# Kernel tuning notes

Measured on AMD Instinct MI355X. Metric: run time of the kernel, lower is better.

Reference implementation:

```python
import jax, jax.numpy as jnp
import numpy as np

HIDDEN = 1024

def setup_inputs() -> dict:
    key = jax.random.key(0)
    ks = jax.random.split(key, 7)
    B, S, H = 4, 4096, HIDDEN
    x = jax.random.normal(ks[0], (B, S, H), dtype=jnp.float32)
    s = 1.0 / np.sqrt(H)
    Wq = jax.random.normal(ks[1], (H, H), dtype=jnp.float32) * s
    bq = jnp.zeros((H,), dtype=jnp.float32)
    Wk = jax.random.normal(ks[2], (H, H), dtype=jnp.float32) * s
    bk = jnp.zeros((H,), dtype=jnp.float32)
    Wv = jax.random.normal(ks[3], (H, H), dtype=jnp.float32) * s
    bv = jnp.zeros((H,), dtype=jnp.float32)
    return {"x": x, "Wq": Wq, "bq": bq, "Wk": Wk, "bk": bk, "Wv": Wv, "bv": bv}

def reference(x, Wq, bq, Wk, bk, Wv, bv):
    # x: [B, S, H]
    scale = jnp.sqrt(jnp.asarray(x.shape[-1], dtype=x.dtype))
    q = jnp.einsum('bsh,hd->bsd', x, Wq) + bq
    k = jnp.einsum('bsh,hd->bsd', x, Wk) + bk
    v = jnp.einsum('bsh,hd->bsd', x, Wv) + bv
    energy = jnp.einsum('bqd,bkd->bqk', q, k) / scale  # [B, S, S]
    attn = jax.nn.softmax(energy, axis=-1)
    return jnp.einsum('bqk,bkd->bqd', attn, v)
```

## Files before the change

### kernel.cpp

```cpp
#include <hip/hip_runtime.h>

typedef unsigned short u16;
typedef __attribute__((ext_vector_type(8))) short short8;
typedef __attribute__((ext_vector_type(4))) short short4v;
typedef __attribute__((ext_vector_type(4))) float floatx4;

#define HD 1024
#define SEQ 4096

__device__ inline u16 f2bf(float f) {
    union { float f; unsigned int i; } c; c.f = f;
    unsigned int r = c.i + 0x7fffu + ((c.i >> 16) & 1u);
    return (u16)(r >> 16);
}

__device__ inline float bf2f(u16 h) {
    union { unsigned int u; float f; } c; c.u = ((unsigned int)h) << 16;
    return c.f;
}

__device__ inline int xcd_chunk(int bid, int nwg) {
    int q = nwg >> 3;
    return (bid & 7) * q + (bid >> 3);
}

__global__ __launch_bounds__(256) void cvt_kernel(const float* __restrict__ in,
                                                  u16* __restrict__ out, int n4) {
    int idx = blockIdx.x * 256 + threadIdx.x;
    int stride = gridDim.x * 256;
    for (int i = idx; i < n4; i += stride) {
        floatx4 v = ((const floatx4*)in)[i];
        short4v o;
        o[0] = (short)f2bf(v[0]); o[1] = (short)f2bf(v[1]);
        o[2] = (short)f2bf(v[2]); o[3] = (short)f2bf(v[3]);
        ((short4v*)out)[i] = o;
    }
}

__global__ __launch_bounds__(256) void wt_kernel(const float* __restrict__ Wq,
                                                 const float* __restrict__ Wk,
                                                 const float* __restrict__ Wv,
                                                 u16* __restrict__ wt) {
    __shared__ u16 tile[64 * 65];
    int z = blockIdx.z;
    const float* W = (z == 0) ? Wq : ((z == 1) ? Wk : Wv);
    u16* out = wt + (size_t)z * HD * HD;
    int k0 = blockIdx.x * 64, n0 = blockIdx.y * 64;
    int t = threadIdx.x;
    int r = t >> 4, c4 = (t & 15) * 4;
    for (int h = 0; h < 4; ++h) {
        int row = r + h * 16;
        floatx4 v = *(const floatx4*)(W + (size_t)(k0 + row) * HD + n0 + c4);
        tile[row * 65 + c4 + 0] = f2bf(v[0]);
        tile[row * 65 + c4 + 1] = f2bf(v[1]);
        tile[row * 65 + c4 + 2] = f2bf(v[2]);
        tile[row * 65 + c4 + 3] = f2bf(v[3]);
    }
    __syncthreads();
    int r2 = t >> 3, c8 = (t & 7) * 8;
    union { short8 v; u16 u[8]; } buf;
    for (int h = 0; h < 2; ++h) {
        int rr = r2 + h * 32;
        #pragma unroll
        for (int i = 0; i < 8; ++i) buf.u[i] = tile[(c8 + i) * 65 + rr];
        *(short8*)(out + (size_t)(n0 + rr) * HD + k0 + c8) = buf.v;
    }
}

__global__ __launch_bounds__(256, 2) void qkv_gemm(const u16* __restrict__ x,
                                                   const u16* __restrict__ wt,
                                                   const float* __restrict__ bq,
                                                   const float* __restrict__ bk,
                                                   const float* __restrict__ bv,
                                                   u16* __restrict__ qb,
                                                   u16* __restrict__ kbuf,
                                                   u16* __restrict__ vtb) {
    __shared__ __align__(16) u16 sA[128 * 32];
    __shared__ __align__(16) u16 sB[128 * 32];
    __shared__ __align__(16) u16 tileC[128 * 132];
    int z = blockIdx.z;
    const u16* Bt = wt + (size_t)z * HD * HD;
    const float* bias = (z == 0) ? bq : ((z == 1) ? bk : bv);
    int m0 = blockIdx.x * 128, n0 = blockIdx.y * 128;
    int t = threadIdx.x, lane = t & 63, w = t >> 6;
    int quad = lane >> 4, l16 = lane & 15;
    int wm = w >> 1, wn = w & 1;
    floatx4 acc[4][4] = {};

    int srow = w * 32 + (lane >> 2);
    int sswz = (lane & 3) ^ ((lane >> 3) & 3);
    const u16* gA = x + (size_t)(m0 + srow) * HD + sswz * 8;
    const u16* gB = Bt + (size_t)(n0 + srow) * HD + sswz * 8;
    u16* lA0 = &sA[(w * 32) * 32];
    u16* lA1 = &sA[(w * 32 + 16) * 32];
    u16* lB0 = &sB[(w * 32) * 32];
    u16* lB1 = &sB[(w * 32 + 16) * 32];

    for (int k0 = 0; k0 < HD; k0 += 32) {
        __builtin_amdgcn_global_load_lds(
            (const __attribute__((address_space(1))) unsigned int*)(const void*)(gA + k0),
            (__attribute__((address_space(3))) unsigned int*)(void*)lA0, 16, 0, 0);
        __builtin_amdgcn_global_load_lds(
            (const __attribute__((address_space(1))) unsigned int*)(const void*)(gA + (size_t)16 * HD + k0),
            (__attribute__((address_space(3))) unsigned int*)(void*)lA1, 16, 0, 0);
        __builtin_amdgcn_global_load_lds(
            (const __attribute__((address_space(1))) unsigned int*)(const void*)(gB + k0),
            (__attribute__((address_space(3))) unsigned int*)(void*)lB0, 16, 0, 0);
        __builtin_amdgcn_global_load_lds(
            (const __attribute__((address_space(1))) unsigned int*)(const void*)(gB + (size_t)16 * HD + k0),
            (__attribute__((address_space(3))) unsigned int*)(void*)lB1, 16, 0, 0);
        __syncthreads();
        short8 af[4], bfr[4];
        #pragma unroll
        for (int i = 0; i < 4; ++i) {
            int ra = wm * 64 + i * 16 + l16;
            af[i] = *(const short8*)&sA[ra * 32 + (quad ^ ((ra >> 1) & 3)) * 8];
        }
        #pragma unroll
        for (int j = 0; j < 4; ++j) {
            int rb = wn * 64 + j * 16 + l16;
            bfr[j] = *(const short8*)&sB[rb * 32 + (quad ^ ((rb >> 1) & 3)) * 8];
        }
        #pragma unroll
        for (int i = 0; i < 4; ++i)
            #pragma unroll
            for (int j = 0; j < 4; ++j)
                acc[i][j] = __builtin_amdgcn_mfma_f32_16x16x32_bf16(af[i], bfr[j], acc[i][j], 0, 0, 0);
        __syncthreads();
    }

    #pragma unroll
    for (int j = 0; j < 4; ++j) {
        int nl = wn * 64 + j * 16 + l16;
        float bb = bias[n0 + nl];
        #pragma unroll
        for (int i = 0; i < 4; ++i) {
            #pragma unroll
            for (int rr = 0; rr < 4; ++rr) {
                int ml = wm * 64 + i * 16 + quad * 4 + rr;
                tileC[ml * 132 + nl] = f2bf(acc[i][j][rr] + bb);
            }
        }
    }
    __syncthreads();
    int r = t >> 1, c0 = (t & 1) * 64;
    if (z != 2) {
        u16* dst = (z == 0) ? qb : kbuf;
        #pragma unroll
        for (int v = 0; v < 8; ++v) {
            short8 vv = *(const short8*)&tileC[r * 132 + c0 + v * 8];
            *(short8*)&dst[(size_t)(m0 + r) * HD + n0 + c0 + v * 8] = vv;
        }
    } else {
        int b_ = m0 >> 12, s0 = m0 & 4095;
        #pragma unroll
        for (int v = 0; v < 8; ++v) {
            union { short8 vv; u16 u[8]; } pk;
            #pragma unroll
            for (int e = 0; e < 8; ++e) pk.u[e] = tileC[(c0 + v * 8 + e) * 132 + r];
            *(short8*)&vtb[((size_t)(b_ * HD + n0 + r)) * SEQ + s0 + c0 + v * 8] = pk.vv;
        }
    }
}

template<int LDA, int LDB, int LDC, int KT, int MT, int NT, bool F32OUT>
__global__ __launch_bounds__(512, 2) void gemm256(const u16* __restrict__ A,
                                                  const u16* __restrict__ B,
                                                  void* __restrict__ C,
                                                  float scale) {
    __shared__ __align__(16) u16 ring[4][2][256 * 32];
    constexpr int NWG = 4 * MT * NT;
    int wg = xcd_chunk(blockIdx.x, NWG);
    int b = wg / (MT * NT);
    int r = wg % (MT * NT);
    int m0 = (r / NT) * 256, n0 = (r % NT) * 256;
    const u16* Ab = A + (size_t)b * MT * 256 * LDA;
    const u16* Bb = B + (size_t)b * NT * 256 * LDB;

    int t = threadIdx.x, lane = t & 63, w = t >> 6;
    int quad = lane >> 4, l16 = lane & 15;
    int wm = w >> 2, wn = w & 3;

    int srow = w * 32 + (lane >> 2);
    int sswz = (lane & 3) ^ ((lane >> 3) & 3);
    const u16* gAs = Ab + (size_t)(m0 + srow) * LDA + sswz * 8;
    const u16* gBs = Bb + (size_t)(n0 + srow) * LDB + sswz * 8;

    auto stage = [&](int kt_) {
        int s_ = kt_ & 3;
        const u16* a0 = gAs + (size_t)kt_ * 32;
        const u16* b0 = gBs + (size_t)kt_ * 32;
        u16* dA = &ring[s_][0][(w * 32) * 32];
        u16* dB = &ring[s_][1][(w * 32) * 32];
        __builtin_amdgcn_global_load_lds(
            (const __attribute__((address_space(1))) unsigned int*)(const void*)a0,
            (__attribute__((address_space(3))) unsigned int*)(void*)dA, 16, 0, 0);
        __builtin_amdgcn_global_load_lds(
            (const __attribute__((address_space(1))) unsigned int*)(const void*)(a0 + (size_t)16 * LDA),
            (__attribute__((address_space(3))) unsigned int*)(void*)(dA + 16 * 32), 16, 0, 0);
        __builtin_amdgcn_global_load_lds(
            (const __attribute__((address_space(1))) unsigned int*)(const void*)b0,
            (__attribute__((address_space(3))) unsigned int*)(void*)dB, 16, 0, 0);
        __builtin_amdgcn_global_load_lds(
            (const __attribute__((address_space(1))) unsigned int*)(const void*)(b0 + (size_t)16 * LDB),
            (__attribute__((address_space(3))) unsigned int*)(void*)(dB + 16 * 32), 16, 0, 0);
    };

    stage(0); stage(1); stage(2);

    floatx4 acc[8][4] = {};

    for (int kt = 0; kt < KT; ++kt) {
        if (kt + 2 < KT)       asm volatile("s_waitcnt vmcnt(8)" ::: "memory");
        else if (kt + 2 == KT) asm volatile("s_waitcnt vmcnt(4)" ::: "memory");
        else                   asm volatile("s_waitcnt vmcnt(0)" ::: "memory");
        __builtin_amdgcn_s_barrier();
        asm volatile("" ::: "memory");
        if (kt + 3 < KT) stage(kt + 3);

        const u16* As = &ring[kt & 3][0][0];
        const u16* Bs = &ring[kt & 3][1][0];
        short8 bf[4], af[8];
        #pragma unroll
        for (int j = 0; j < 4; ++j) {
            int rb = wn * 64 + j * 16 + l16;
            bf[j] = *(const short8*)&Bs[rb * 32 + (quad ^ ((rb >> 1) & 3)) * 8];
        }
        #pragma unroll
        for (int i = 0; i < 8; ++i) {
            int ra = wm * 128 + i * 16 + l16;
            af[i] = *(const short8*)&As[ra * 32 + (quad ^ ((ra >> 1) & 3)) * 8];
        }
        __builtin_amdgcn_s_setprio(1);
        #pragma unroll
        for (int i = 0; i < 8; ++i)
            #pragma unroll
            for (int j = 0; j < 4; ++j)
                acc[i][j] = __builtin_amdgcn_mfma_f32_16x16x32_bf16(af[i], bf[j], acc[i][j], 0, 0, 0);
        __builtin_amdgcn_s_setprio(0);
    }

    if constexpr (F32OUT) {
        float* Cb = (float*)C + (size_t)b * MT * 256 * LDC;
        #pragma unroll
        for (int i = 0; i < 8; ++i)
            #pragma unroll
            for (int rr = 0; rr < 4; ++rr) {
                int m = m0 + wm * 128 + i * 16 + quad * 4 + rr;
                float* row = Cb + (size_t)m * LDC + n0 + wn * 64 + l16;
                #pragma unroll
                for (int j = 0; j < 4; ++j)
                    row[j * 16] = acc[i][j][rr] * scale;
            }
    } else {
        u16* Cb = (u16*)C + (size_t)b * MT * 256 * LDC;
        #pragma unroll
        for (int i = 0; i < 8; ++i)
            #pragma unroll
            for (int rr = 0; rr < 4; ++rr) {
                int m = m0 + wm * 128 + i * 16 + quad * 4 + rr;
                u16* row = Cb + (size_t)m * LDC + n0 + wn * 64 + l16;
                #pragma unroll
                for (int j = 0; j < 4; ++j)
                    row[j * 16] = f2bf(acc[i][j][rr] * scale);
            }
    }
}

__global__ __launch_bounds__(256) void softmax_kernel(u16* __restrict__ S) {
    int w = threadIdx.x >> 6, lane = threadIdx.x & 63;
    size_t row = (size_t)blockIdx.x * 4 + w;
    u16* p = S + row * SEQ;
    float sv[64];
    float mx = -1e30f;
    #pragma unroll
    for (int c = 0; c < 8; ++c) {
        short8 v = *(const short8*)&p[(c * 64 + lane) * 8];
        #pragma unroll
        for (int e = 0; e < 8; ++e) {
            float f = bf2f((u16)v[e]);
            sv[c * 8 + e] = f;
            mx = fmaxf(mx, f);
        }
    }
    mx = fmaxf(mx, __shfl_xor(mx, 1));
    mx = fmaxf(mx, __shfl_xor(mx, 2));
    mx = fmaxf(mx, __shfl_xor(mx, 4));
    mx = fmaxf(mx, __shfl_xor(mx, 8));
    mx = fmaxf(mx, __shfl_xor(mx, 16));
    mx = fmaxf(mx, __shfl_xor(mx, 32));
    float sum = 0.f;
    #pragma unroll
    for (int i = 0; i < 64; ++i) { sv[i] = __expf(sv[i] - mx); sum += sv[i]; }
    sum += __shfl_xor(sum, 1);
    sum += __shfl_xor(sum, 2);
    sum += __shfl_xor(sum, 4);
    sum += __shfl_xor(sum, 8);
    sum += __shfl_xor(sum, 16);
    sum += __shfl_xor(sum, 32);
    float rinv = 1.f / sum;
    #pragma unroll
    for (int c = 0; c < 8; ++c) {
        union { short8 vv; u16 u[8]; } o;
        #pragma unroll
        for (int e = 0; e < 8; ++e) o.u[e] = f2bf(sv[c * 8 + e] * rinv);
        *(short8*)&p[(c * 64 + lane) * 8] = o.vv;
    }
}

__global__ __launch_bounds__(512, 2) void flash_kernel(const u16* __restrict__ q,
                                                       const u16* __restrict__ k,
                                                       const u16* __restrict__ vt,
                                                       float* __restrict__ out) {
    __shared__ __align__(16) u16 q_lds[64 * 1032];
    __shared__ float Sc[64 * 66];
    __shared__ __align__(16) u16 Pb[64 * 72];
    __shared__ float m_st[64], l_st[64], al_st[64];

    int t = threadIdx.x, lane = t & 63, w = t >> 6;
    int quad = lane >> 4, l16 = lane & 15;
    int j = w & 3, hh = w >> 2;
    int bid = blockIdx.x;
    int xcd = bid & 7;
    int b = xcd >> 1;
    int q0 = (((bid >> 3) << 1) + (xcd & 1)) * 64;

    for (int i = t; i < 64 * 128; i += 512) {
        int r = i >> 7, c8 = (i & 127) * 8;
        *(short8*)&q_lds[r * 1032 + c8] =
            *(const short8*)&q[((size_t)(b * SEQ + q0 + r)) * HD + c8];
    }
    if (t < 64) { m_st[t] = -1e30f; l_st[t] = 0.f; }
    floatx4 o_acc[4][8] = {};
    __syncthreads();

    const u16* kwave = k + ((size_t)(b * SEQ + j * 16 + l16)) * HD + hh * 512 + quad * 8;
    const u16* vwave = vt + ((size_t)(b * HD + w * 128 + l16)) * SEQ + quad * 8;
    int r2 = t >> 3;
    int cg = (t & 7) * 8;

    for (int tt = 0; tt < 64; ++tt) {
        int kb = tt * 64;
        floatx4 s_acc[4] = {};
        const u16* kp = kwave + (size_t)kb * HD;
        #pragma unroll 8
        for (int ks = 0; ks < 16; ++ks) {
            short8 kf = *(const short8*)(kp + ks * 32);
            #pragma unroll
            for (int rb = 0; rb < 4; ++rb) {
                short8 qf = *(const short8*)&q_lds[(rb * 16 + l16) * 1032 + hh * 512 + ks * 32 + quad * 8];
                s_acc[rb] = __builtin_amdgcn_mfma_f32_16x16x32_bf16(qf, kf, s_acc[rb], 0, 0, 0);
            }
        }
        if (hh == 0) {
            #pragma unroll
            for (int rb = 0; rb < 4; ++rb)
                #pragma unroll
                for (int rr = 0; rr < 4; ++rr)
                    Sc[(rb * 16 + quad * 4 + rr) * 66 + j * 16 + l16] = s_acc[rb][rr] * 0.03125f;
        }
        __syncthreads();
        if (hh == 1) {
            #pragma unroll
            for (int rb = 0; rb < 4; ++rb)
                #pragma unroll
                for (int rr = 0; rr < 4; ++rr)
                    Sc[(rb * 16 + quad * 4 + rr) * 66 + j * 16 + l16] += s_acc[rb][rr] * 0.03125f;
        }
        __syncthreads();

        float sv[8];
        float mloc = -1e30f;
        #pragma unroll
        for (int i = 0; i < 8; ++i) { sv[i] = Sc[r2 * 66 + cg + i]; mloc = fmaxf(mloc, sv[i]); }
        mloc = fmaxf(mloc, __shfl_xor(mloc, 1));
        mloc = fmaxf(mloc, __shfl_xor(mloc, 2));
        mloc = fmaxf(mloc, __shfl_xor(mloc, 4));
        float m_old = m_st[r2];
        float m_new = fmaxf(m_old, mloc);
        float alpha = __expf(m_old - m_new);
        float sum = 0.f;
        #pragma unroll
        for (int i = 0; i < 8; ++i) {
            float p = __expf(sv[i] - m_new);
            sum += p;
            Pb[r2 * 72 + cg + i] = f2bf(p);
        }
        sum += __shfl_xor(sum, 1);
        sum += __shfl_xor(sum, 2);
        sum += __shfl_xor(sum, 4);
        if ((t & 7) == 0) {
            m_st[r2] = m_new;
            l_st[r2] = l_st[r2] * alpha + sum;
            al_st[r2] = alpha;
        }
        __syncthreads();

        #pragma unroll
        for (int rb = 0; rb < 4; ++rb) {
            float a0 = al_st[rb * 16 + quad * 4 + 0];
            float a1 = al_st[rb * 16 + quad * 4 + 1];
            float a2 = al_st[rb * 16 + quad * 4 + 2];
            float a3 = al_st[rb * 16 + quad * 4 + 3];
            #pragma unroll
            for (int dt = 0; dt < 8; ++dt) {
                o_acc[rb][dt][0] *= a0;
                o_acc[rb][dt][1] *= a1;
                o_acc[rb][dt][2] *= a2;
                o_acc[rb][dt][3] *= a3;
            }
        }
        short8 pf[4][2];
        #pragma unroll
        for (int rb = 0; rb < 4; ++rb)
            #pragma unroll
            for (int ks2 = 0; ks2 < 2; ++ks2)
                pf[rb][ks2] = *(const short8*)&Pb[(rb * 16 + l16) * 72 + ks2 * 32 + quad * 8];
        const u16* vp = vwave + kb;
        #pragma unroll
        for (int dt = 0; dt < 8; ++dt) {
            short8 vf0 = *(const short8*)(vp + (size_t)dt * 16 * SEQ);
            short8 vf1 = *(const short8*)(vp + (size_t)dt * 16 * SEQ + 32);
            #pragma unroll
            for (int rb = 0; rb < 4; ++rb) {
                o_acc[rb][dt] = __builtin_amdgcn_mfma_f32_16x16x32_bf16(pf[rb][0], vf0, o_acc[rb][dt], 0, 0, 0);
                o_acc[rb][dt] = __builtin_amdgcn_mfma_f32_16x16x32_bf16(pf[rb][1], vf1, o_acc[rb][dt], 0, 0, 0);
            }
        }
    }

    #pragma unroll
    for (int rb = 0; rb < 4; ++rb) {
        #pragma unroll
        for (int rr = 0; rr < 4; ++rr) {
            int row = rb * 16 + quad * 4 + rr;
            float linv = 1.f / l_st[row];
            #pragma unroll
            for (int dt = 0; dt < 8; ++dt) {
                out[((size_t)(b * SEQ + q0 + row)) * HD + w * 128 + dt * 16 + l16] =
                    o_acc[rb][dt][rr] * linv;
            }
        }
    }
}

extern "C" void kernel_launch(void* const* d_in, const int* in_sizes, int n_in,
                              void* d_out, int out_size, void* d_ws, size_t ws_size,
                              hipStream_t stream) {
    const float* x  = (const float*)d_in[0];
    const float* Wq = (const float*)d_in[1];
    const float* bq = (const float*)d_in[2];
    const float* Wk = (const float*)d_in[3];
    const float* bk = (const float*)d_in[4];
    const float* Wv = (const float*)d_in[5];
    const float* bv = (const float*)d_in[6];
    float* out = (float*)d_out;
    char* ws = (char*)d_ws;
    const size_t MB = 1024 * 1024;

    if (ws_size >= 224 * MB) {
        u16* vtb = (u16*)ws;
        u16* qb  = (u16*)(ws + 32 * MB);
        u16* kb  = (u16*)(ws + 64 * MB);
        u16* S   = (u16*)(ws + 96 * MB);
        u16* xb  = (u16*)(ws + 96 * MB);
        u16* wt  = (u16*)(ws + 128 * MB);

        cvt_kernel<<<dim3(4096), 256, 0, stream>>>(x, xb, (4 * SEQ * HD) / 4);
        wt_kernel<<<dim3(16, 16, 3), 256, 0, stream>>>(Wq, Wk, Wv, wt);
        qkv_gemm<<<dim3(128, 8, 3), 256, 0, stream>>>(xb, wt, bq, bk, bv, qb, kb, vtb);
        gemm256<HD, HD, SEQ, 32, 16, 16, false><<<dim3(1024), 512, 0, stream>>>(qb, kb, S, 0.03125f);
        softmax_kernel<<<dim3(4096), 256, 0, stream>>>(S);
        gemm256<SEQ, SEQ, HD, 128, 16, 4, true><<<dim3(256), 512, 0, stream>>>(S, vtb, out, 1.0f);
    } else {
        u16* xb  = (u16*)ws;
        u16* wt  = (u16*)(ws + 32 * MB);
        u16* qb  = (u16*)(ws + 38 * MB);
        u16* kb  = (u16*)(ws + 70 * MB);
        u16* vtb = (u16*)(ws + 102 * MB);

        cvt_kernel<<<dim3(4096), 256, 0, stream>>>(x, xb, (4 * SEQ * HD) / 4);
        wt_kernel<<<dim3(16, 16, 3), 256, 0, stream>>>(Wq, Wk, Wv, wt);
        qkv_gemm<<<dim3(128, 8, 3), 256, 0, stream>>>(xb, wt, bq, bk, bv, qb, kb, vtb);
        flash_kernel<<<dim3(256), 512, 0, stream>>>(qb, kb, vtb, out);
    }
}
```

Measured before the change: 568.4 us.

## Split QKV projection into 256x256 pipelined Q/K kernel and separate V kernel

```diff
diff --git a/kernel.cpp b/kernel.cpp
--- a/kernel.cpp
+++ b/kernel.cpp
@@ -64,6 +64,180 @@
         #pragma unroll
         for (int i = 0; i < 8; ++i) buf.u[i] = tile[(c8 + i) * 65 + rr];
         *(short8*)(out + (size_t)(n0 + rr) * HD + k0 + c8) = buf.v;
+    }
+}
+
+__global__ __launch_bounds__(512, 2) void qkv256(const u16* __restrict__ x,
+                                                 const u16* __restrict__ wt,
+                                                 const float* __restrict__ bq,
+                                                 const float* __restrict__ bk,
+                                                 u16* __restrict__ qb,
+                                                 u16* __restrict__ kbuf) {
+    __shared__ __align__(16) u16 ring[4][2][256 * 32];
+    int wg = xcd_chunk(blockIdx.x, 512);
+    int z = wg >> 8;
+    int r = wg & 255;
+    int m0 = (r >> 2) * 256, n0 = (r & 3) * 256;
+    const u16* Bb = wt + (size_t)z * HD * HD;
+    const float* bias = z ? bk : bq;
+    u16* C = z ? kbuf : qb;
+
+    int t = threadIdx.x, lane = t & 63, w = t >> 6;
+    int quad = lane >> 4, l16 = lane & 15;
+    int wm = w >> 2, wn = w & 3;
+
+    int srow = w * 32 + (lane >> 2);
+    int sswz = (lane & 3) ^ ((lane >> 3) & 3);
+    const u16* gAs = x + (size_t)(m0 + srow) * HD + sswz * 8;
+    const u16* gBs = Bb + (size_t)(n0 + srow) * HD + sswz * 8;
+
+    auto stage = [&](int kt_) {
+        int s_ = kt_ & 3;
+        const u16* a0 = gAs + (size_t)kt_ * 32;
+        const u16* b0 = gBs + (size_t)kt_ * 32;
+        u16* dA = &ring[s_][0][(w * 32) * 32];
+        u16* dB = &ring[s_][1][(w * 32) * 32];
+        __builtin_amdgcn_global_load_lds(
+            (const __attribute__((address_space(1))) unsigned int*)(const void*)a0,
+            (__attribute__((address_space(3))) unsigned int*)(void*)dA, 16, 0, 0);
+        __builtin_amdgcn_global_load_lds(
+            (const __attribute__((address_space(1))) unsigned int*)(const void*)(a0 + (size_t)16 * HD),
+            (__attribute__((address_space(3))) unsigned int*)(void*)(dA + 16 * 32), 16, 0, 0);
+        __builtin_amdgcn_global_load_lds(
+            (const __attribute__((address_space(1))) unsigned int*)(const void*)b0,
+            (__attribute__((address_space(3))) unsigned int*)(void*)dB, 16, 0, 0);
+        __builtin_amdgcn_global_load_lds(
+            (const __attribute__((address_space(1))) unsigned int*)(const void*)(b0 + (size_t)16 * HD),
+            (__attribute__((address_space(3))) unsigned int*)(void*)(dB + 16 * 32), 16, 0, 0);
+    };
+
+    stage(0); stage(1); stage(2);
+
+    floatx4 acc[8][4] = {};
+    constexpr int KT = HD / 32;
+
+    for (int kt = 0; kt < KT; ++kt) {
+        if (kt + 2 < KT)       asm volatile("s_waitcnt vmcnt(8)" ::: "memory");
+        else if (kt + 2 == KT) asm volatile("s_waitcnt vmcnt(4)" ::: "memory");
+        else                   asm volatile("s_waitcnt vmcnt(0)" ::: "memory");
+        __builtin_amdgcn_s_barrier();
+        asm volatile("" ::: "memory");
+        if (kt + 3 < KT) stage(kt + 3);
+
+        const u16* As = &ring[kt & 3][0][0];
+        const u16* Bs = &ring[kt & 3][1][0];
+        short8 bf[4], af[8];
+        #pragma unroll
+        for (int j = 0; j < 4; ++j) {
+            int rb = wn * 64 + j * 16 + l16;
+            bf[j] = *(const short8*)&Bs[rb * 32 + (quad ^ ((rb >> 1) & 3)) * 8];
+        }
+        #pragma unroll
+        for (int i = 0; i < 8; ++i) {
+            int ra = wm * 128 + i * 16 + l16;
+            af[i] = *(const short8*)&As[ra * 32 + (quad ^ ((ra >> 1) & 3)) * 8];
+        }
+        __builtin_amdgcn_s_setprio(1);
+        #pragma unroll
+        for (int i = 0; i < 8; ++i)
+            #pragma unroll
+            for (int j = 0; j < 4; ++j)
+                acc[i][j] = __builtin_amdgcn_mfma_f32_16x16x32_bf16(af[i], bf[j], acc[i][j], 0, 0, 0);
+        __builtin_amdgcn_s_setprio(0);
+    }
+
+    float bb[4];
+    #pragma unroll
+    for (int j = 0; j < 4; ++j) bb[j] = bias[n0 + wn * 64 + j * 16 + l16];
+    #pragma unroll
+    for (int i = 0; i < 8; ++i)
+        #pragma unroll
+        for (int rr = 0; rr < 4; ++rr) {
+            int m = m0 + wm * 128 + i * 16 + quad * 4 + rr;
+            u16* row = C + (size_t)m * HD + n0 + wn * 64 + l16;
+            #pragma unroll
+            for (int j = 0; j < 4; ++j)
+                row[j * 16] = f2bf(acc[i][j][rr] + bb[j]);
+        }
+}
+
+__global__ __launch_bounds__(256, 2) void v_gemm(const u16* __restrict__ x,
+                                                 const u16* __restrict__ wtv,
+                                                 const float* __restrict__ bv,
+                                                 u16* __restrict__ vtb) {
+    __shared__ __align__(16) u16 sA[128 * 32];
+    __shared__ __align__(16) u16 sB[128 * 32];
+    __shared__ __align__(16) u16 tileC[128 * 132];
+    int m0 = blockIdx.x * 128, n0 = blockIdx.y * 128;
+    int t = threadIdx.x, lane = t & 63, w = t >> 6;
+    int quad = lane >> 4, l16 = lane & 15;
+    int wm = w >> 1, wn = w & 1;
+    floatx4 acc[4][4] = {};
+
+    int srow = w * 32 + (lane >> 2);
+    int sswz = (lane & 3) ^ ((lane >> 3) & 3);
+    const u16* gA = x + (size_t)(m0 + srow) * HD + sswz * 8;
+    const u16* gB = wtv + (size_t)(n0 + srow) * HD + sswz * 8;
+    u16* lA0 = &sA[(w * 32) * 32];
+    u16* lA1 = &sA[(w * 32 + 16) * 32];
+    u16* lB0 = &sB[(w * 32) * 32];
+    u16* lB1 = &sB[(w * 32 + 16) * 32];
+
+    for (int k0 = 0; k0 < HD; k0 += 32) {
+        __builtin_amdgcn_global_load_lds(
+            (const __attribute__((address_space(1))) unsigned int*)(const void*)(gA + k0),
+            (__attribute__((address_space(3))) unsigned int*)(void*)lA0, 16, 0, 0);
+        __builtin_amdgcn_global_load_lds(
+            (const __attribute__((address_space(1))) unsigned int*)(const void*)(gA + (size_t)16 * HD + k0),
+            (__attribute__((address_space(3))) unsigned int*)(void*)lA1, 16, 0, 0);
+        __builtin_amdgcn_global_load_lds(
+            (const __attribute__((address_space(1))) unsigned int*)(const void*)(gB + k0),
+            (__attribute__((address_space(3))) unsigned int*)(void*)lB0, 16, 0, 0);
+        __builtin_amdgcn_global_load_lds(
+            (const __attribute__((address_space(1))) unsigned int*)(const void*)(gB + (size_t)16 * HD + k0),
+            (__attribute__((address_space(3))) unsigned int*)(void*)lB1, 16, 0, 0);
+        __syncthreads();
+        short8 af[4], bfr[4];
+        #pragma unroll
+        for (int i = 0; i < 4; ++i) {
+            int ra = wm * 64 + i * 16 + l16;
+            af[i] = *(const short8*)&sA[ra * 32 + (quad ^ ((ra >> 1) & 3)) * 8];
+        }
+        #pragma unroll
+        for (int j = 0; j < 4; ++j) {
+            int rb = wn * 64 + j * 16 + l16;
+            bfr[j] = *(const short8*)&sB[rb * 32 + (quad ^ ((rb >> 1) & 3)) * 8];
+        }
+        #pragma unroll
+        for (int i = 0; i < 4; ++i)
+            #pragma unroll
+            for (int j = 0; j < 4; ++j)
+                acc[i][j] = __builtin_amdgcn_mfma_f32_16x16x32_bf16(af[i], bfr[j], acc[i][j], 0, 0, 0);
+        __syncthreads();
+    }
+
+    #pragma unroll
+    for (int j = 0; j < 4; ++j) {
+        int nl = wn * 64 + j * 16 + l16;
+        float bb = bv[n0 + nl];
+        #pragma unroll
+        for (int i = 0; i < 4; ++i) {
+            #pragma unroll
+            for (int rr = 0; rr < 4; ++rr) {
+                int ml = wm * 64 + i * 16 + quad * 4 + rr;
+                tileC[ml * 132 + nl] = f2bf(acc[i][j][rr] + bb);
+            }
+        }
+    }
+    __syncthreads();
+    int r = t >> 1, c0 = (t & 1) * 64;
+    int b_ = m0 >> 12, s0 = m0 & 4095;
+    #pragma unroll
+    for (int v = 0; v < 8; ++v) {
+        union { short8 vv; u16 u[8]; } pk;
+        #pragma unroll
+        for (int e = 0; e < 8; ++e) pk.u[e] = tileC[(c0 + v * 8 + e) * 132 + r];
+        *(short8*)&vtb[((size_t)(b_ * HD + n0 + r)) * SEQ + s0 + c0 + v * 8] = pk.vv;
     }
 }
 
@@ -468,7 +642,8 @@
 
         cvt_kernel<<<dim3(4096), 256, 0, stream>>>(x, xb, (4 * SEQ * HD) / 4);
         wt_kernel<<<dim3(16, 16, 3), 256, 0, stream>>>(Wq, Wk, Wv, wt);
-        qkv_gemm<<<dim3(128, 8, 3), 256, 0, stream>>>(xb, wt, bq, bk, bv, qb, kb, vtb);
+        qkv256<<<dim3(512), 512, 0, stream>>>(xb, wt, bq, bk, qb, kb);
+        v_gemm<<<dim3(128, 8), 256, 0, stream>>>(xb, wt + (size_t)2 * HD * HD, bv, vtb);
         gemm256<HD, HD, SEQ, 32, 16, 16, false><<<dim3(1024), 512, 0, stream>>>(qb, kb, S, 0.03125f);
         softmax_kernel<<<dim3(4096), 256, 0, stream>>>(S);
         gemm256<SEQ, SEQ, HD, 128, 16, 4, true><<<dim3(256), 512, 0, stream>>>(S, vtb, out, 1.0f);
```

Measured after the change: 548.4 us. 1.04x faster.

## Rework gemm256 to BK=64 double-buffer with interleaved fragment loads; split QK projection

Applied to the files above, without the earlier changes.

```diff
diff --git a/kernel.cpp b/kernel.cpp
--- a/kernel.cpp
+++ b/kernel.cpp
@@ -22,6 +22,12 @@
 __device__ inline int xcd_chunk(int bid, int nwg) {
     int q = nwg >> 3;
     return (bid & 7) * q + (bid >> 3);
+}
+
+__device__ inline void glds16(const u16* g, u16* l) {
+    __builtin_amdgcn_global_load_lds(
+        (const __attribute__((address_space(1))) unsigned int*)(const void*)g,
+        (__attribute__((address_space(3))) unsigned int*)(void*)l, 16, 0, 0);
 }
 
 __global__ __launch_bounds__(256) void cvt_kernel(const float* __restrict__ in,
@@ -64,6 +70,214 @@
         #pragma unroll
         for (int i = 0; i < 8; ++i) buf.u[i] = tile[(c8 + i) * 65 + rr];
         *(short8*)(out + (size_t)(n0 + rr) * HD + k0 + c8) = buf.v;
+    }
+}
+
+#define RD_A(i, ks) (*(const short8*)&As[(wm * 128 + (i) * 16 + l16) * 64 + ((((ks) * 4 + quad)) ^ (l16 & 7)) * 8])
+#define RD_B(j, ks) (*(const short8*)&Bs[(wn * 64 + (j) * 16 + l16) * 64 + ((((ks) * 4 + quad)) ^ (l16 & 7)) * 8])
+
+#define GEMM256_CORE(KTN, LDA_, LDB_)                                                   \
+    int t = threadIdx.x, lane = t & 63, w = t >> 6;                                     \
+    int quad = lane >> 4, l16 = lane & 15;                                              \
+    int wm = w >> 2, wn = w & 3;                                                        \
+    int l8r = lane >> 3;                                                                \
+    int sswz = (lane & 7) ^ l8r;                                                        \
+    const u16* gAs = Ab + (size_t)(m0 + w * 32 + l8r) * LDA_ + sswz * 8;                \
+    const u16* gBs = Bb + (size_t)(n0 + w * 32 + l8r) * LDB_ + sswz * 8;                \
+    auto stage = [&](int kt_) {                                                         \
+        int s_ = kt_ & 1;                                                               \
+        const u16* a0 = gAs + (size_t)kt_ * 64;                                         \
+        const u16* b0 = gBs + (size_t)kt_ * 64;                                         \
+        _Pragma("unroll")                                                               \
+        for (int L = 0; L < 4; ++L) {                                                   \
+            glds16(a0 + (size_t)(8 * L) * LDA_, &ring[s_][0][(w * 32 + 8 * L) * 64]);   \
+            glds16(b0 + (size_t)(8 * L) * LDB_, &ring[s_][1][(w * 32 + 8 * L) * 64]);   \
+        }                                                                               \
+    };                                                                                  \
+    floatx4 acc[8][4] = {};                                                             \
+    stage(0);                                                                           \
+    for (int kt = 0; kt < (KTN); ++kt) {                                                \
+        asm volatile("s_waitcnt vmcnt(0)" ::: "memory");        \
+        __builtin_amdgcn_s_barrier();                         \
+        asm volatile("" ::: "memory");                                                  \
+        if (kt + 1 < (KTN)) stage(kt + 1);      \
+        const u16* As = &ring[kt & 1][0][0];                                            \
+        const u16* Bs = &ring[kt & 1][1][0];                                            \
+        short8 bfr[2][4];                                                               \
+        short8 afr[2][2];                                                               \
+        _Pragma("unroll")                                                               \
+        for (int j = 0; j < 4; ++j) bfr[0][j] = RD_B(j, 0);                             \
+        afr[0][0] = RD_A(0, 0);                                                         \
+        afr[0][1] = RD_A(1, 0);                                                         \
+        _Pragma("unroll")                                                               \
+        for (int p = 0; p < 8; ++p) {                                                   \
+            int ks = p >> 2, q = p & 3;                                                 \
+            int cur = p & 1, nxt = cur ^ 1;                                             \
+            if (p < 7) {                                                                \
+                int pn = p + 1;                                                         \
+                int ksn = pn >> 2, qn = pn & 3;                                         \
+                if (qn == 0) {                                                          \
+                    _Pragma("unroll")                                                   \
+                    for (int j = 0; j < 4; ++j) bfr[1][j] = RD_B(j, 1);                 \
+                }                                                                       \
+                afr[nxt][0] = RD_A(2 * qn, ksn);                                        \
+                afr[nxt][1] = RD_A(2 * qn + 1, ksn);                                    \
+            }                                                                           \
+            __builtin_amdgcn_s_setprio(1);                                              \
+            _Pragma("unroll")                                                           \
+            for (int j = 0; j < 4; ++j) {                                               \
+                acc[2 * q][j] = __builtin_amdgcn_mfma_f32_16x16x32_bf16(afr[cur][0], bfr[ks][j], acc[2 * q][j], 0, 0, 0);       \
+                acc[2 * q + 1][j] = __builtin_amdgcn_mfma_f32_16x16x32_bf16(afr[cur][1], bfr[ks][j], acc[2 * q + 1][j], 0, 0, 0); \
+            }                                                                           \
+            __builtin_amdgcn_s_setprio(0);                                              \
+        }                                                                               \
+    }
+
+template<int LDA, int LDB, int LDC, int KT, int MT, int NT, bool F32OUT>
+__global__ __launch_bounds__(512, 2) void gemm256(const u16* __restrict__ A,
+                                                  const u16* __restrict__ B,
+                                                  void* __restrict__ C,
+                                                  float scale) {
+    __shared__ __align__(16) u16 ring[2][2][256 * 64];
+    constexpr int NWG = 4 * MT * NT;
+    int wg = xcd_chunk(blockIdx.x, NWG);
+    int b = wg / (MT * NT);
+    int r = wg % (MT * NT);
+    int m0 = (r / NT) * 256, n0 = (r % NT) * 256;
+    const u16* Ab = A + (size_t)b * MT * 256 * LDA;
+    const u16* Bb = B + (size_t)b * NT * 256 * LDB;
+
+    GEMM256_CORE(KT, LDA, LDB)
+
+    if constexpr (F32OUT) {
+        float* Cb = (float*)C + (size_t)b * MT * 256 * LDC;
+        #pragma unroll
+        for (int i = 0; i < 8; ++i)
+            #pragma unroll
+            for (int rr = 0; rr < 4; ++rr) {
+                int m = m0 + wm * 128 + i * 16 + quad * 4 + rr;
+                float* row = Cb + (size_t)m * LDC + n0 + wn * 64 + l16;
+                #pragma unroll
+                for (int j = 0; j < 4; ++j)
+                    row[j * 16] = acc[i][j][rr] * scale;
+            }
+    } else {
+        u16* Cb = (u16*)C + (size_t)b * MT * 256 * LDC;
+        #pragma unroll
+        for (int i = 0; i < 8; ++i)
+            #pragma unroll
+            for (int rr = 0; rr < 4; ++rr) {
+                int m = m0 + wm * 128 + i * 16 + quad * 4 + rr;
+                u16* row = Cb + (size_t)m * LDC + n0 + wn * 64 + l16;
+                #pragma unroll
+                for (int j = 0; j < 4; ++j)
+                    row[j * 16] = f2bf(acc[i][j][rr] * scale);
+            }
+    }
+}
+
+__global__ __launch_bounds__(512, 2) void qkv256(const u16* __restrict__ x,
+                                                 const u16* __restrict__ wt,
+                                                 const float* __restrict__ bq,
+                                                 const float* __restrict__ bk,
+                                                 u16* __restrict__ qb,
+                                                 u16* __restrict__ kbuf) {
+    __shared__ __align__(16) u16 ring[2][2][256 * 64];
+    int wg = xcd_chunk(blockIdx.x, 512);
+    int z = wg >> 8;
+    int r = wg & 255;
+    int m0 = (r >> 2) * 256, n0 = (r & 3) * 256;
+    const u16* Ab = x;
+    const u16* Bb = wt + (size_t)z * HD * HD;
+    const float* bias = z ? bk : bq;
+    u16* C = z ? kbuf : qb;
+
+    GEMM256_CORE(16, HD, HD)
+
+    float bb[4];
+    #pragma unroll
+    for (int j = 0; j < 4; ++j) bb[j] = bias[n0 + wn * 64 + j * 16 + l16];
+    #pragma unroll
+    for (int i = 0; i < 8; ++i)
+        #pragma unroll
+        for (int rr = 0; rr < 4; ++rr) {
+            int m = m0 + wm * 128 + i * 16 + quad * 4 + rr;
+            u16* row = C + (size_t)m * HD + n0 + wn * 64 + l16;
+            #pragma unroll
+            for (int j = 0; j < 4; ++j)
+                row[j * 16] = f2bf(acc[i][j][rr] + bb[j]);
+        }
+}
+
+__global__ __launch_bounds__(256, 2) void v_gemm(const u16* __restrict__ x,
+                                                 const u16* __restrict__ wtv,
+                                                 const float* __restrict__ bv,
+                                                 u16* __restrict__ vtb) {
+    __shared__ __align__(16) u16 sA[128 * 32];
+    __shared__ __align__(16) u16 sB[128 * 32];
+    __shared__ __align__(16) u16 tileC[128 * 132];
+    int m0 = blockIdx.x * 128, n0 = blockIdx.y * 128;
+    int t = threadIdx.x, lane = t & 63, w = t >> 6;
+    int quad = lane >> 4, l16 = lane & 15;
+    int wm = w >> 1, wn = w & 1;
+    floatx4 acc[4][4] = {};
+
+    int srow = w * 32 + (lane >> 2);
+    int sswz = (lane & 3) ^ ((lane >> 3) & 3);
+    const u16* gA = x + (size_t)(m0 + srow) * HD + sswz * 8;
+    const u16* gB = wtv + (size_t)(n0 + srow) * HD + sswz * 8;
+    u16* lA0 = &sA[(w * 32) * 32];
+    u16* lA1 = &sA[(w * 32 + 16) * 32];
+    u16* lB0 = &sB[(w * 32) * 32];
+    u16* lB1 = &sB[(w * 32 + 16) * 32];
+
+    for (int k0 = 0; k0 < HD; k0 += 32) {
+        glds16(gA + k0, lA0);
+        glds16(gA + (size_t)16 * HD + k0, lA1);
+        glds16(gB + k0, lB0);
+        glds16(gB + (size_t)16 * HD + k0, lB1);
+        __syncthreads();
+        short8 af[4], bfr[4];
+        #pragma unroll
+        for (int i = 0; i < 4; ++i) {
+            int ra = wm * 64 + i * 16 + l16;
+            af[i] = *(const short8*)&sA[ra * 32 + (quad ^ ((ra >> 1) & 3)) * 8];
+        }
+        #pragma unroll
+        for (int j = 0; j < 4; ++j) {
+            int rb = wn * 64 + j * 16 + l16;
+            bfr[j] = *(const short8*)&sB[rb * 32 + (quad ^ ((rb >> 1) & 3)) * 8];
+        }
+        #pragma unroll
+        for (int i = 0; i < 4; ++i)
+            #pragma unroll
+            for (int j = 0; j < 4; ++j)
+                acc[i][j] = __builtin_amdgcn_mfma_f32_16x16x32_bf16(af[i], bfr[j], acc[i][j], 0, 0, 0);
+        __syncthreads();
+    }
+
+    #pragma unroll
+    for (int j = 0; j < 4; ++j) {
+        int nl = wn * 64 + j * 16 + l16;
+        float bb = bv[n0 + nl];
+        #pragma unroll
+        for (int i = 0; i < 4; ++i) {
+            #pragma unroll
+            for (int rr = 0; rr < 4; ++rr) {
+                int ml = wm * 64 + i * 16 + quad * 4 + rr;
+                tileC[ml * 132 + nl] = f2bf(acc[i][j][rr] + bb);
+            }
+        }
+    }
+    __syncthreads();
+    int r = t >> 1, c0 = (t & 1) * 64;
+    int b_ = m0 >> 12, s0 = m0 & 4095;
+    #pragma unroll
+    for (int v = 0; v < 8; ++v) {
+        union { short8 vv; u16 u[8]; } pk;
+        #pragma unroll
+        for (int e = 0; e < 8; ++e) pk.u[e] = tileC[(c0 + v * 8 + e) * 132 + r];
+        *(short8*)&vtb[((size_t)(b_ * HD + n0 + r)) * SEQ + s0 + c0 + v * 8] = pk.vv;
     }
 }
 
@@ -97,18 +311,10 @@
     u16* lB1 = &sB[(w * 32 + 16) * 32];
 
     for (int k0 = 0; k0 < HD; k0 += 32) {
-        __builtin_amdgcn_global_load_lds(
-            (const __attribute__((address_space(1))) unsigned int*)(const void*)(gA + k0),
-            (__attribute__((address_space(3))) unsigned int*)(void*)lA0, 16, 0, 0);
-        __builtin_amdgcn_global_load_lds(
-            (const __attribute__((address_space(1))) unsigned int*)(const void*)(gA + (size_t)16 * HD + k0),
-            (__attribute__((address_space(3))) unsigned int*)(void*)lA1, 16, 0, 0);
-        __builtin_amdgcn_global_load_lds(
-            (const __attribute__((address_space(1))) unsigned int*)(const void*)(gB + k0),
-            (__attribute__((address_space(3))) unsigned int*)(void*)lB0, 16, 0, 0);
-        __builtin_amdgcn_global_load_lds(
-            (const __attribute__((address_space(1))) unsigned int*)(const void*)(gB + (size_t)16 * HD + k0),
-            (__attribute__((address_space(3))) unsigned int*)(void*)lB1, 16, 0, 0);
+        glds16(gA + k0, lA0);
+        glds16(gA + (size_t)16 * HD + k0, lA1);
+        glds16(gB + k0, lB0);
+        glds16(gB + (size_t)16 * HD + k0, lB1);
         __syncthreads();
         short8 af[4], bfr[4];
         #pragma unroll
@@ -160,110 +366,6 @@
             for (int e = 0; e < 8; ++e) pk.u[e] = tileC[(c0 + v * 8 + e) * 132 + r];
             *(short8*)&vtb[((size_t)(b_ * HD + n0 + r)) * SEQ + s0 + c0 + v * 8] = pk.vv;
         }
-    }
-}
-
-template<int LDA, int LDB, int LDC, int KT, int MT, int NT, bool F32OUT>
-__global__ __launch_bounds__(512, 2) void gemm256(const u16* __restrict__ A,
-                                                  const u16* __restrict__ B,
-                                                  void* __restrict__ C,
-                                                  float scale) {
-    __shared__ __align__(16) u16 ring[4][2][256 * 32];
-    constexpr int NWG = 4 * MT * NT;
-    int wg = xcd_chunk(blockIdx.x, NWG);
-    int b = wg / (MT * NT);
-    int r = wg % (MT * NT);
-    int m0 = (r / NT) * 256, n0 = (r % NT) * 256;
-    const u16* Ab = A + (size_t)b * MT * 256 * LDA;
-    const u16* Bb = B + (size_t)b * NT * 256 * LDB;
-
-    int t = threadIdx.x, lane = t & 63, w = t >> 6;
-    int quad = lane >> 4, l16 = lane & 15;
-    int wm = w >> 2, wn = w & 3;
-
-    int srow = w * 32 + (lane >> 2);
-    int sswz = (lane & 3) ^ ((lane >> 3) & 3);
-    const u16* gAs = Ab + (size_t)(m0 + srow) * LDA + sswz * 8;
-    const u16* gBs = Bb + (size_t)(n0 + srow) * LDB + sswz * 8;
-
-    auto stage = [&](int kt_) {
-        int s_ = kt_ & 3;
-        const u16* a0 = gAs + (size_t)kt_ * 32;
-        const u16* b0 = gBs + (size_t)kt_ * 32;
-        u16* dA = &ring[s_][0][(w * 32) * 32];
-        u16* dB = &ring[s_][1][(w * 32) * 32];
-        __builtin_amdgcn_global_load_lds(
-            (const __attribute__((address_space(1))) unsigned int*)(const void*)a0,
-            (__attribute__((address_space(3))) unsigned int*)(void*)dA, 16, 0, 0);
-        __builtin_amdgcn_global_load_lds(
-            (const __attribute__((address_space(1))) unsigned int*)(const void*)(a0 + (size_t)16 * LDA),
-            (__attribute__((address_space(3))) unsigned int*)(void*)(dA + 16 * 32), 16, 0, 0);
-        __builtin_amdgcn_global_load_lds(
-            (const __attribute__((address_space(1))) unsigned int*)(const void*)b0,
-            (__attribute__((address_space(3))) unsigned int*)(void*)dB, 16, 0, 0);
-        __builtin_amdgcn_global_load_lds(
-            (const __attribute__((address_space(1))) unsigned int*)(const void*)(b0 + (size_t)16 * LDB),
-            (__attribute__((address_space(3))) unsigned int*)(void*)(dB + 16 * 32), 16, 0, 0);
-    };
-
-    stage(0); stage(1); stage(2);
-
-    floatx4 acc[8][4] = {};
-
-    for (int kt = 0; kt < KT; ++kt) {
-        if (kt + 2 < KT)       asm volatile("s_waitcnt vmcnt(8)" ::: "memory");
-        else if (kt + 2 == KT) asm volatile("s_waitcnt vmcnt(4)" ::: "memory");
-        else                   asm volatile("s_waitcnt vmcnt(0)" ::: "memory");
-        __builtin_amdgcn_s_barrier();
-        asm volatile("" ::: "memory");
-        if (kt + 3 < KT) stage(kt + 3);
-
-        const u16* As = &ring[kt & 3][0][0];
-        const u16* Bs = &ring[kt & 3][1][0];
-        short8 bf[4], af[8];
-        #pragma unroll
-        for (int j = 0; j < 4; ++j) {
-            int rb = wn * 64 + j * 16 + l16;
-            bf[j] = *(const short8*)&Bs[rb * 32 + (quad ^ ((rb >> 1) & 3)) * 8];
-        }
-        #pragma unroll
-        for (int i = 0; i < 8; ++i) {
-            int ra = wm * 128 + i * 16 + l16;
-            af[i] = *(const short8*)&As[ra * 32 + (quad ^ ((ra >> 1) & 3)) * 8];
-        }
-        __builtin_amdgcn_s_setprio(1);
-        #pragma unroll
-        for (int i = 0; i < 8; ++i)
-            #pragma unroll
-            for (int j = 0; j < 4; ++j)
-                acc[i][j] = __builtin_amdgcn_mfma_f32_16x16x32_bf16(af[i], bf[j], acc[i][j], 0, 0, 0);
-        __builtin_amdgcn_s_setprio(0);
-    }
-
-    if constexpr (F32OUT) {
-        float* Cb = (float*)C + (size_t)b * MT * 256 * LDC;
-        #pragma unroll
-        for (int i = 0; i < 8; ++i)
-            #pragma unroll
-            for (int rr = 0; rr < 4; ++rr) {
-                int m = m0 + wm * 128 + i * 16 + quad * 4 + rr;
-                float* row = Cb + (size_t)m * LDC + n0 + wn * 64 + l16;
-                #pragma unroll
-                for (int j = 0; j < 4; ++j)
-                    row[j * 16] = acc[i][j][rr] * scale;
-            }
-    } else {
-        u16* Cb = (u16*)C + (size_t)b * MT * 256 * LDC;
-        #pragma unroll
-        for (int i = 0; i < 8; ++i)
-            #pragma unroll
-            for (int rr = 0; rr < 4; ++rr) {
-                int m = m0 + wm * 128 + i * 16 + quad * 4 + rr;
-                u16* row = Cb + (size_t)m * LDC + n0 + wn * 64 + l16;
-                #pragma unroll
-                for (int j = 0; j < 4; ++j)
-                    row[j * 16] = f2bf(acc[i][j][rr] * scale);
-            }
     }
 }
 
@@ -468,10 +570,11 @@
 
         cvt_kernel<<<dim3(4096), 256, 0, stream>>>(x, xb, (4 * SEQ * HD) / 4);
         wt_kernel<<<dim3(16, 16, 3), 256, 0, stream>>>(Wq, Wk, Wv, wt);
-        qkv_gemm<<<dim3(128, 8, 3), 256, 0, stream>>>(xb, wt, bq, bk, bv, qb, kb, vtb);
-        gemm256<HD, HD, SEQ, 32, 16, 16, false><<<dim3(1024), 512, 0, stream>>>(qb, kb, S, 0.03125f);
+        qkv256<<<dim3(512), 512, 0, stream>>>(xb, wt, bq, bk, qb, kb);
+        v_gemm<<<dim3(128, 8), 256, 0, stream>>>(xb, wt + (size_t)2 * HD * HD, bv, vtb);
+        gemm256<HD, HD, SEQ, 16, 16, 16, false><<<dim3(1024), 512, 0, stream>>>(qb, kb, S, 0.03125f);
         softmax_kernel<<<dim3(4096), 256, 0, stream>>>(S);
-        gemm256<SEQ, SEQ, HD, 128, 16, 4, true><<<dim3(256), 512, 0, stream>>>(S, vtb, out, 1.0f);
+        gemm256<SEQ, SEQ, HD, 64, 16, 4, true><<<dim3(256), 512, 0, stream>>>(S, vtb, out, 1.0f);
     } else {
         u16* xb  = (u16*)ws;
         u16* wt  = (u16*)(ws + 32 * MB);
```

New measurement: 504.9 us. 1.13x faster.
